# Optimization experiments

Hardware: AMD Instinct MI355X
Metric: run time of the kernel (lower is better)

## Reference

```python
import jax, jax.numpy as jnp
import numpy as np

BETA = 0.25


def setup_inputs() -> dict:
    key = jax.random.key(0)
    k1, k2 = jax.random.split(key)
    B, W, H, C = 32, 64, 64, 64
    K = 512
    x = jax.random.normal(k1, (B, W, H, C), dtype=jnp.float32)
    # original uses random_uniform_initializer(0, 1)
    embedding = jax.random.uniform(k2, (K, C), dtype=jnp.float32)
    return {"x": x, "embedding": embedding}


def reference(x, embedding):
    B, W, H, C = x.shape
    K = embedding.shape[0]
    flat = x.reshape(-1, C)  # (N, C), N = B*W*H
    # squared L2 distance, expanded form (same math as sum((flat - emb)^2, -1))
    # avoids materializing the (N, K, C) tiled tensor of the original
    x2 = jnp.sum(flat * flat, axis=-1, keepdims=True)          # (N, 1)
    e2 = jnp.sum(embedding * embedding, axis=-1)               # (K,)
    cross = jnp.einsum('nc,kc->nk', flat, embedding)           # (N, K)
    dist = x2 - 2.0 * cross + e2[None, :]                      # (N, K)
    idx = jnp.argmin(dist, axis=-1).reshape(B, W, H)           # (B, W, H)
    quantized = embedding[idx]                                 # (B, W, H, C)
    embedding_loss = jnp.mean((jax.lax.stop_gradient(x) - quantized) ** 2)
    encoding_loss = jnp.mean((x - jax.lax.stop_gradient(quantized)) ** 2)
    loss = embedding_loss + BETA * encoding_loss
    # straight-through estimator
    quantized_ste = x + jax.lax.stop_gradient(quantized - x)
    return quantized_ste, loss
```

## Files before the change

### kernel.cpp

```cpp
#include <hip/hip_runtime.h>


#define C_DIM 64
#define K_EMB 512
#define KCH   (K_EMB / 2)
#define NVEC (32 * 64 * 64)
#define BLK 512
#define NPB 256
#define GRID (NVEC / NPB)
#define KTC 16
#define NT 2

typedef __attribute__((ext_vector_type(8))) short bf16x8;
typedef __attribute__((ext_vector_type(4))) float f32x4;

#define WS_E2   0
#define WS_EHI  4096
#define WS_ELO  (4096 + 65536)
#define WS_PART (4096 + 2 * 65536)

__device__ inline unsigned short f2bf(float f) {
    unsigned u = __float_as_uint(f);
    u += 0x7FFF + ((u >> 16) & 1);
    return (unsigned short)(u >> 16);
}
__device__ inline float bf2f(unsigned short h) {
    return __uint_as_float(((unsigned)h) << 16);
}
__device__ inline bool lessidx(float s, int i, float t, int j) {
    return (s < t) || (s == t && i < j);
}

__global__ __launch_bounds__(512) void vq_prep(const float* __restrict__ emb,
                                               float* __restrict__ e2,
                                               short* __restrict__ ehi,
                                               short* __restrict__ elo) {
    const int t = blockIdx.x * 512 + threadIdx.x;
    const int l = t & 63;
    const int kt2 = t >> 6;
    const int row = (kt2 >> 1) * 16 + (l & 15);
    const int cb  = (kt2 & 1) * 32 + (l >> 4) * 8;
    const float* src = emb + row * C_DIM + cb;
    bf16x8 vh, vl;
#pragma unroll
    for (int j = 0; j < 8; ++j) {
        float v = -2.0f * src[j];
        unsigned short h = f2bf(v);
        float hf = bf2f(h);
        unsigned short q = f2bf(v - hf);
        vh[j] = (short)h;
        vl[j] = (short)q;
    }
    *(bf16x8*)(ehi + (size_t)t * 8) = vh;
    *(bf16x8*)(elo + (size_t)t * 8) = vl;

    if (t < K_EMB) {
        const float* r = emb + t * C_DIM;
        float s = 0.f;
#pragma unroll
        for (int c = 0; c < C_DIM; ++c) s += r[c] * r[c];
        e2[t] = s;
    }
}

__global__ __launch_bounds__(BLK, 4) void vq_main(
    const float* __restrict__ x,
    const float* __restrict__ emb,
    const float* __restrict__ e2g,
    const short* __restrict__ ehi_g,
    const short* __restrict__ elo_g,
    float* __restrict__ out,
    double* __restrict__ partials)
{
    __shared__ __align__(16) short s_hi[KCH * C_DIM];
    __shared__ __align__(16) short s_lo[KCH * C_DIM];
    __shared__ __align__(16) float s_e2[K_EMB];
    __shared__ double s_wsum[BLK / 64];

    const int tid  = threadIdx.x;
    const int lane = tid & 63;
    const int wid  = tid >> 6;
    const int lr   = lane & 15;
    const int lh   = lane >> 4;
    const int nbase = blockIdx.x * NPB + wid * 32;

    float4 xr[8];
#pragma unroll
    for (int nt = 0; nt < NT; ++nt) {
        const float* xp = x + (size_t)(nbase + nt * 16 + lr) * C_DIM;
#pragma unroll
        for (int s = 0; s < 2; ++s) {
            xr[nt * 4 + s * 2 + 0] = *(const float4*)(xp + s * 32 + lh * 8);
            xr[nt * 4 + s * 2 + 1] = *(const float4*)(xp + s * 32 + lh * 8 + 4);
        }
    }

    if (tid < K_EMB) s_e2[tid] = e2g[tid];
    {
        const float4* srch = (const float4*)ehi_g;
        const float4* srcl = (const float4*)elo_g;
        float4* dsth = (float4*)s_hi;
        float4* dstl = (float4*)s_lo;
#pragma unroll
        for (int i = 0; i < 4; ++i) dsth[tid + i * BLK] = srch[tid + i * BLK];
#pragma unroll
        for (int i = 0; i < 4; ++i) dstl[tid + i * BLK] = srcl[tid + i * BLK];
    }
    __syncthreads();

    bf16x8 xh[NT][2], xl[NT][2];
    float x2p[NT];
#pragma unroll
    for (int nt = 0; nt < NT; ++nt) {
        x2p[nt] = 0.f;
#pragma unroll
        for (int s = 0; s < 2; ++s) {
            float4 a = xr[nt * 4 + s * 2 + 0];
            float4 b = xr[nt * 4 + s * 2 + 1];
            float vv[8] = {a.x, a.y, a.z, a.w, b.x, b.y, b.z, b.w};
#pragma unroll
            for (int j = 0; j < 8; ++j) {
                float v = vv[j];
                x2p[nt] += v * v;
                unsigned short h = f2bf(v);
                float hf = bf2f(h);
                unsigned short q = f2bf(v - hf);
                xh[nt][s][j] = (short)h;
                xl[nt][s][j] = (short)q;
            }
        }
    }

    float pb1[NT] = {1e30f, 1e30f}, pb2[NT] = {1e30f, 1e30f};

#pragma unroll 1
    for (int ch = 0; ch < 2; ++ch) {
        if (ch == 1) {
            __syncthreads();
            const float4* srch = (const float4*)ehi_g + 2048;
            const float4* srcl = (const float4*)elo_g + 2048;
            float4* dsth = (float4*)s_hi;
            float4* dstl = (float4*)s_lo;
#pragma unroll
            for (int i = 0; i < 4; ++i) dsth[tid + i * BLK] = srch[tid + i * BLK];
#pragma unroll
            for (int i = 0; i < 4; ++i) dstl[tid + i * BLK] = srcl[tid + i * BLK];
            __syncthreads();
        }
        const int ktb = ch * KTC;
        const bf16x8* hb = (const bf16x8*)s_hi + lane;
        const bf16x8* lb = (const bf16x8*)s_lo + lane;

#pragma unroll 2
        for (int kt = 0; kt < KTC; ++kt) {
            bf16x8 ah0 = hb[kt * 128], ah1 = hb[kt * 128 + 64];
            bf16x8 al0 = lb[kt * 128], al1 = lb[kt * 128 + 64];
            float4 ev = *(const float4*)(s_e2 + (ktb + kt) * 16 + lh * 4);

            f32x4 h0 = {ev.x, ev.y, ev.z, ev.w};
            f32x4 h1 = h0;
            f32x4 p0 = {0.f, 0.f, 0.f, 0.f};
            f32x4 p1 = p0, q0 = p0, q1 = p0;

            h0 = __builtin_amdgcn_mfma_f32_16x16x32_bf16(ah0, xh[0][0], h0, 0, 0, 0);
            h1 = __builtin_amdgcn_mfma_f32_16x16x32_bf16(ah0, xh[1][0], h1, 0, 0, 0);
            p0 = __builtin_amdgcn_mfma_f32_16x16x32_bf16(al0, xh[0][0], p0, 0, 0, 0);
            p1 = __builtin_amdgcn_mfma_f32_16x16x32_bf16(al0, xh[1][0], p1, 0, 0, 0);
            q0 = __builtin_amdgcn_mfma_f32_16x16x32_bf16(ah0, xl[0][0], q0, 0, 0, 0);
            q1 = __builtin_amdgcn_mfma_f32_16x16x32_bf16(ah0, xl[1][0], q1, 0, 0, 0);
            h0 = __builtin_amdgcn_mfma_f32_16x16x32_bf16(ah1, xh[0][1], h0, 0, 0, 0);
            h1 = __builtin_amdgcn_mfma_f32_16x16x32_bf16(ah1, xh[1][1], h1, 0, 0, 0);
            p0 = __builtin_amdgcn_mfma_f32_16x16x32_bf16(al1, xh[0][1], p0, 0, 0, 0);
            p1 = __builtin_amdgcn_mfma_f32_16x16x32_bf16(al1, xh[1][1], p1, 0, 0, 0);
            q0 = __builtin_amdgcn_mfma_f32_16x16x32_bf16(ah1, xl[0][1], q0, 0, 0, 0);
            q1 = __builtin_amdgcn_mfma_f32_16x16x32_bf16(ah1, xl[1][1], q1, 0, 0, 0);

            f32x4 s0 = (h0 + p0) + q0;
            f32x4 s1 = (h1 + p1) + q1;

            const unsigned kb4 = (unsigned)((ktb + kt) * 4);
#define PACKMIN(ACC, NTI)                                                          \
            {                                                                      \
                unsigned u0 = ((__float_as_uint(ACC[0]) + 64u) & 0xFFFFFF80u) | (kb4 + 0); \
                unsigned u1 = ((__float_as_uint(ACC[1]) + 64u) & 0xFFFFFF80u) | (kb4 + 1); \
                unsigned u2 = ((__float_as_uint(ACC[2]) + 64u) & 0xFFFFFF80u) | (kb4 + 2); \
                unsigned u3 = ((__float_as_uint(ACC[3]) + 64u) & 0xFFFFFF80u) | (kb4 + 3); \
                float f0 = __uint_as_float(u0), f1 = __uint_as_float(u1);          \
                float f2 = __uint_as_float(u2), f3 = __uint_as_float(u3);          \
                float lo = fminf(f0, f1), hi = fmaxf(f0, f1);                      \
                pb2[NTI] = fminf(fminf(pb2[NTI], fmaxf(pb1[NTI], lo)), hi);        \
                pb1[NTI] = fminf(pb1[NTI], lo);                                    \
                lo = fminf(f2, f3); hi = fmaxf(f2, f3);                            \
                pb2[NTI] = fminf(fminf(pb2[NTI], fmaxf(pb1[NTI], lo)), hi);        \
                pb1[NTI] = fminf(pb1[NTI], lo);                                    \
            }
            PACKMIN(s0, 0)
            PACKMIN(s1, 1)
#undef PACKMIN
        }
    }

    double dsum = 0.0;
#pragma unroll
    for (int nt = 0; nt < NT; ++nt) {
        unsigned u1 = __float_as_uint(pb1[nt]);
        unsigned u2 = __float_as_uint(pb2[nt]);
        int loc1 = u1 & 127, loc2 = u2 & 127;
        float b1 = __uint_as_float(u1 & 0xFFFFFF80u);
        float b2 = __uint_as_float(u2 & 0xFFFFFF80u);
        int i1 = ((loc1 >> 2) << 4) + lh * 4 + (loc1 & 3);
        int i2 = ((loc2 >> 2) << 4) + lh * 4 + (loc2 & 3);
        float xx = x2p[nt];
#pragma unroll
        for (int off = 16; off <= 32; off <<= 1) {
            float ob1 = __shfl_xor(b1, off, 64);
            int   oi1 = __shfl_xor(i1, off, 64);
            float ob2 = __shfl_xor(b2, off, 64);
            int   oi2 = __shfl_xor(i2, off, 64);
            float oxx = __shfl_xor(xx, off, 64);
            xx += oxx;
            bool to = lessidx(ob1, oi1, b1, i1);
            float w1 = to ? ob1 : b1;  int wi1 = to ? oi1 : i1;
            float l1 = to ? b1 : ob1;  int li1 = to ? i1 : oi1;
            float c2 = to ? ob2 : b2;  int ci2 = to ? oi2 : i2;
            bool t2 = lessidx(l1, li1, c2, ci2);
            b1 = w1; i1 = wi1;
            b2 = t2 ? l1 : c2; i2 = t2 ? li1 : ci2;
        }

        int bw = i1;
        if (lane < 16) {
            double md;
            if (b2 - b1 < 1.2e-2f) {
                const int n = nbase + nt * 16 + lane;
                const float4* xq = (const float4*)(x + (size_t)n * C_DIM);
                const float4* p1 = (const float4*)(emb + (size_t)i1 * C_DIM);
                const float4* p2 = (const float4*)(emb + (size_t)i2 * C_DIM);
                double s1 = 0.0, s2 = 0.0;
#pragma unroll
                for (int i = 0; i < 16; ++i) {
                    float4 xv = xq[i]; float4 a = p1[i]; float4 bq = p2[i];
                    double d;
                    d = (double)xv.x - (double)a.x;  s1 = fma(d, d, s1);
                    d = (double)xv.y - (double)a.y;  s1 = fma(d, d, s1);
                    d = (double)xv.z - (double)a.z;  s1 = fma(d, d, s1);
                    d = (double)xv.w - (double)a.w;  s1 = fma(d, d, s1);
                    d = (double)xv.x - (double)bq.x; s2 = fma(d, d, s2);
                    d = (double)xv.y - (double)bq.y; s2 = fma(d, d, s2);
                    d = (double)xv.z - (double)bq.z; s2 = fma(d, d, s2);
                    d = (double)xv.w - (double)bq.w; s2 = fma(d, d, s2);
                }
                if (s2 < s1 || (s1 == s2 && i2 < i1)) { bw = i2; md = s2; }
                else                                   { md = s1; }
            } else {
                md = (double)xx + (double)b1;
            }
            dsum += md;
        }

        {
            const int v  = lane >> 2;
            const int c0 = lane & 3;
            const int w  = __shfl(bw, v);
            const size_t rowb = ((size_t)(nbase + nt * 16 + v)) * 16;
            const float4* ep = (const float4*)emb + (size_t)w * 16;
            float4* op = (float4*)out;
#pragma unroll
            for (int it = 0; it < 4; ++it) op[rowb + c0 + it * 4] = ep[c0 + it * 4];
        }
    }

#pragma unroll
    for (int off = 1; off <= 8; off <<= 1) dsum += __shfl_xor(dsum, off, 64);
    if (lane == 0) s_wsum[wid] = dsum;
    __syncthreads();
    if (tid == 0) {
        double t = 0.0;
#pragma unroll
        for (int i = 0; i < BLK / 64; ++i) t += s_wsum[i];
        partials[blockIdx.x] = t;
    }
}

__global__ __launch_bounds__(512) void vq_finalize(const double* __restrict__ partials,
                                                   float* __restrict__ out) {
    double v = partials[threadIdx.x];
#pragma unroll
    for (int off = 32; off; off >>= 1) v += __shfl_down(v, off, 64);
    __shared__ double ls[8];
    const int lane = threadIdx.x & 63;
    const int wid  = threadIdx.x >> 6;
    if (lane == 0) ls[wid] = v;
    __syncthreads();
    if (threadIdx.x == 0) {
        double t = 0.0;
#pragma unroll
        for (int i = 0; i < 8; ++i) t += ls[i];
        double mean = t / (double)((size_t)NVEC * C_DIM);
        out[(size_t)NVEC * C_DIM] = (float)(1.25 * mean);
    }
}

extern "C" void kernel_launch(void* const* d_in, const int* in_sizes, int n_in,
                              void* d_out, int out_size, void* d_ws, size_t ws_size,
                              hipStream_t stream) {
    const float* x   = (const float*)d_in[0];
    const float* emb = (const float*)d_in[1];
    float* out = (float*)d_out;

    float*  e2       = (float*)((char*)d_ws + WS_E2);
    short*  ehi      = (short*)((char*)d_ws + WS_EHI);
    short*  elo      = (short*)((char*)d_ws + WS_ELO);
    double* partials = (double*)((char*)d_ws + WS_PART);

    vq_prep<<<8, 512, 0, stream>>>(emb, e2, ehi, elo);
    vq_main<<<GRID, BLK, 0, stream>>>(x, emb, e2, ehi, elo, out, partials);
    vq_finalize<<<1, 512, 0, stream>>>(partials, out);
}
```

Baseline: 53.19 us.

## Switch to fp16 split-x MFMA with single embedding copy and larger per-wave tile

The codebook is now a single fp16 copy of -2*emb kept entirely in LDS, replacing the bf16 hi/lo pair that was loaded in two chunks. Only x is split into hi and lo halves, which cuts the MFMAs per tile from 3 products to 2. Each wave now covers 64 vectors (NT=4) and blocks drop to 256 threads, so embedding fragments are reused across more MFMAs and the mid-kernel resync and reload go away. The near-tie fallback is widened and now runs in parallel across lanes with fp64 distances, to make up for fp16 losing exponent range and precision. This costs 64KB of LDS per block, which lowers occupancy, and a wider fallback window sends more vectors down the exact path.

```diff
diff --git a/kernel.cpp b/kernel.cpp
--- a/kernel.cpp
+++ b/kernel.cpp
@@ -3,56 +3,55 @@
 
 #define C_DIM 64
 #define K_EMB 512
-#define KCH   (K_EMB / 2)
 #define NVEC (32 * 64 * 64)
-#define BLK 512
+#define BLK 256
+#define VPW 64
 #define NPB 256
 #define GRID (NVEC / NPB)
-#define KTC 16
-#define NT 2
-
-typedef __attribute__((ext_vector_type(8))) short bf16x8;
+#define KT (K_EMB / 16)
+#define NT 4
+#define WINF 2.5e-2f
+
+typedef __attribute__((ext_vector_type(8))) _Float16 f16x8;
 typedef __attribute__((ext_vector_type(4))) float f32x4;
 
 #define WS_E2   0
-#define WS_EHI  4096
-#define WS_ELO  (4096 + 65536)
-#define WS_PART (4096 + 2 * 65536)
-
-__device__ inline unsigned short f2bf(float f) {
-    unsigned u = __float_as_uint(f);
-    u += 0x7FFF + ((u >> 16) & 1);
-    return (unsigned short)(u >> 16);
-}
-__device__ inline float bf2f(unsigned short h) {
-    return __uint_as_float(((unsigned)h) << 16);
-}
+#define WS_AE   4096
+#define WS_PART (4096 + 65536)
+
 __device__ inline bool lessidx(float s, int i, float t, int j) {
     return (s < t) || (s == t && i < j);
 }
 
+__device__ __forceinline__ double dist64(const float4* __restrict__ xq,
+                                         const float* __restrict__ ep) {
+    const float4* e4 = (const float4*)ep;
+    double s = 0.0;
+#pragma unroll
+    for (int i = 0; i < 16; ++i) {
+        float4 xv = xq[i]; float4 a = e4[i];
+        double d;
+        d = (double)xv.x - (double)a.x; s = fma(d, d, s);
+        d = (double)xv.y - (double)a.y; s = fma(d, d, s);
+        d = (double)xv.z - (double)a.z; s = fma(d, d, s);
+        d = (double)xv.w - (double)a.w; s = fma(d, d, s);
+    }
+    return s;
+}
+
 __global__ __launch_bounds__(512) void vq_prep(const float* __restrict__ emb,
                                                float* __restrict__ e2,
-                                               short* __restrict__ ehi,
-                                               short* __restrict__ elo) {
+                                               short* __restrict__ ae) {
     const int t = blockIdx.x * 512 + threadIdx.x;
     const int l = t & 63;
     const int kt2 = t >> 6;
     const int row = (kt2 >> 1) * 16 + (l & 15);
     const int cb  = (kt2 & 1) * 32 + (l >> 4) * 8;
     const float* src = emb + row * C_DIM + cb;
-    bf16x8 vh, vl;
-#pragma unroll
-    for (int j = 0; j < 8; ++j) {
-        float v = -2.0f * src[j];
-        unsigned short h = f2bf(v);
-        float hf = bf2f(h);
-        unsigned short q = f2bf(v - hf);
-        vh[j] = (short)h;
-        vl[j] = (short)q;
-    }
-    *(bf16x8*)(ehi + (size_t)t * 8) = vh;
-    *(bf16x8*)(elo + (size_t)t * 8) = vl;
+    f16x8 vh;
+#pragma unroll
+    for (int j = 0; j < 8; ++j) vh[j] = (_Float16)(-2.0f * src[j]);
+    *(f16x8*)(ae + (size_t)t * 8) = vh;
 
     if (t < K_EMB) {
         const float* r = emb + t * C_DIM;
@@ -63,17 +62,15 @@
     }
 }
 
-__global__ __launch_bounds__(BLK, 4) void vq_main(
+__global__ __launch_bounds__(BLK, 2) void vq_main(
     const float* __restrict__ x,
     const float* __restrict__ emb,
     const float* __restrict__ e2g,
-    const short* __restrict__ ehi_g,
-    const short* __restrict__ elo_g,
+    const short* __restrict__ ae_g,
     float* __restrict__ out,
     double* __restrict__ partials)
 {
-    __shared__ __align__(16) short s_hi[KCH * C_DIM];
-    __shared__ __align__(16) short s_lo[KCH * C_DIM];
+    __shared__ __align__(16) short s_ae[K_EMB * C_DIM];
     __shared__ __align__(16) float s_e2[K_EMB];
     __shared__ double s_wsum[BLK / 64];
 
@@ -82,9 +79,9 @@
     const int wid  = tid >> 6;
     const int lr   = lane & 15;
     const int lh   = lane >> 4;
-    const int nbase = blockIdx.x * NPB + wid * 32;
-
-    float4 xr[8];
+    const int nbase = blockIdx.x * NPB + wid * VPW;
+
+    float4 xr[NT * 4];
 #pragma unroll
     for (int nt = 0; nt < NT; ++nt) {
         const float* xp = x + (size_t)(nbase + nt * 16 + lr) * C_DIM;
@@ -95,20 +92,17 @@
         }
     }
 
-    if (tid < K_EMB) s_e2[tid] = e2g[tid];
     {
-        const float4* srch = (const float4*)ehi_g;
-        const float4* srcl = (const float4*)elo_g;
-        float4* dsth = (float4*)s_hi;
-        float4* dstl = (float4*)s_lo;
-#pragma unroll
-        for (int i = 0; i < 4; ++i) dsth[tid + i * BLK] = srch[tid + i * BLK];
-#pragma unroll
-        for (int i = 0; i < 4; ++i) dstl[tid + i * BLK] = srcl[tid + i * BLK];
+        const float4* srca = (const float4*)ae_g;
+        float4* dsta = (float4*)s_ae;
+#pragma unroll
+        for (int i = 0; i < 16; ++i) dsta[tid + i * BLK] = srca[tid + i * BLK];
+        s_e2[tid] = e2g[tid];
+        s_e2[tid + 256] = e2g[tid + 256];
     }
     __syncthreads();
 
-    bf16x8 xh[NT][2], xl[NT][2];
+    f16x8 xh[NT][2], xl[NT][2];
     float x2p[NT];
 #pragma unroll
     for (int nt = 0; nt < NT; ++nt) {
@@ -122,81 +116,52 @@
             for (int j = 0; j < 8; ++j) {
                 float v = vv[j];
                 x2p[nt] += v * v;
-                unsigned short h = f2bf(v);
-                float hf = bf2f(h);
-                unsigned short q = f2bf(v - hf);
-                xh[nt][s][j] = (short)h;
-                xl[nt][s][j] = (short)q;
+                _Float16 h = (_Float16)v;
+                xh[nt][s][j] = h;
+                xl[nt][s][j] = (_Float16)(v - (float)h);
             }
         }
     }
 
-    float pb1[NT] = {1e30f, 1e30f}, pb2[NT] = {1e30f, 1e30f};
-
-#pragma unroll 1
-    for (int ch = 0; ch < 2; ++ch) {
-        if (ch == 1) {
-            __syncthreads();
-            const float4* srch = (const float4*)ehi_g + 2048;
-            const float4* srcl = (const float4*)elo_g + 2048;
-            float4* dsth = (float4*)s_hi;
-            float4* dstl = (float4*)s_lo;
-#pragma unroll
-            for (int i = 0; i < 4; ++i) dsth[tid + i * BLK] = srch[tid + i * BLK];
-#pragma unroll
-            for (int i = 0; i < 4; ++i) dstl[tid + i * BLK] = srcl[tid + i * BLK];
-            __syncthreads();
-        }
-        const int ktb = ch * KTC;
-        const bf16x8* hb = (const bf16x8*)s_hi + lane;
-        const bf16x8* lb = (const bf16x8*)s_lo + lane;
+    float pb1[NT] = {1e30f, 1e30f, 1e30f, 1e30f};
+    float pb2[NT] = {1e30f, 1e30f, 1e30f, 1e30f};
+    const f16x8* ab = (const f16x8*)s_ae + lane;
 
 #pragma unroll 2
-        for (int kt = 0; kt < KTC; ++kt) {
-            bf16x8 ah0 = hb[kt * 128], ah1 = hb[kt * 128 + 64];
-            bf16x8 al0 = lb[kt * 128], al1 = lb[kt * 128 + 64];
-            float4 ev = *(const float4*)(s_e2 + (ktb + kt) * 16 + lh * 4);
-
-            f32x4 h0 = {ev.x, ev.y, ev.z, ev.w};
-            f32x4 h1 = h0;
-            f32x4 p0 = {0.f, 0.f, 0.f, 0.f};
-            f32x4 p1 = p0, q0 = p0, q1 = p0;
-
-            h0 = __builtin_amdgcn_mfma_f32_16x16x32_bf16(ah0, xh[0][0], h0, 0, 0, 0);
-            h1 = __builtin_amdgcn_mfma_f32_16x16x32_bf16(ah0, xh[1][0], h1, 0, 0, 0);
-            p0 = __builtin_amdgcn_mfma_f32_16x16x32_bf16(al0, xh[0][0], p0, 0, 0, 0);
-            p1 = __builtin_amdgcn_mfma_f32_16x16x32_bf16(al0, xh[1][0], p1, 0, 0, 0);
-            q0 = __builtin_amdgcn_mfma_f32_16x16x32_bf16(ah0, xl[0][0], q0, 0, 0, 0);
-            q1 = __builtin_amdgcn_mfma_f32_16x16x32_bf16(ah0, xl[1][0], q1, 0, 0, 0);
-            h0 = __builtin_amdgcn_mfma_f32_16x16x32_bf16(ah1, xh[0][1], h0, 0, 0, 0);
-            h1 = __builtin_amdgcn_mfma_f32_16x16x32_bf16(ah1, xh[1][1], h1, 0, 0, 0);
-            p0 = __builtin_amdgcn_mfma_f32_16x16x32_bf16(al1, xh[0][1], p0, 0, 0, 0);
-            p1 = __builtin_amdgcn_mfma_f32_16x16x32_bf16(al1, xh[1][1], p1, 0, 0, 0);
-            q0 = __builtin_amdgcn_mfma_f32_16x16x32_bf16(ah1, xl[0][1], q0, 0, 0, 0);
-            q1 = __builtin_amdgcn_mfma_f32_16x16x32_bf16(ah1, xl[1][1], q1, 0, 0, 0);
-
-            f32x4 s0 = (h0 + p0) + q0;
-            f32x4 s1 = (h1 + p1) + q1;
-
-            const unsigned kb4 = (unsigned)((ktb + kt) * 4);
-#define PACKMIN(ACC, NTI)                                                          \
-            {                                                                      \
-                unsigned u0 = ((__float_as_uint(ACC[0]) + 64u) & 0xFFFFFF80u) | (kb4 + 0); \
-                unsigned u1 = ((__float_as_uint(ACC[1]) + 64u) & 0xFFFFFF80u) | (kb4 + 1); \
-                unsigned u2 = ((__float_as_uint(ACC[2]) + 64u) & 0xFFFFFF80u) | (kb4 + 2); \
-                unsigned u3 = ((__float_as_uint(ACC[3]) + 64u) & 0xFFFFFF80u) | (kb4 + 3); \
-                float f0 = __uint_as_float(u0), f1 = __uint_as_float(u1);          \
-                float f2 = __uint_as_float(u2), f3 = __uint_as_float(u3);          \
-                float lo = fminf(f0, f1), hi = fmaxf(f0, f1);                      \
-                pb2[NTI] = fminf(fminf(pb2[NTI], fmaxf(pb1[NTI], lo)), hi);        \
-                pb1[NTI] = fminf(pb1[NTI], lo);                                    \
-                lo = fminf(f2, f3); hi = fmaxf(f2, f3);                            \
-                pb2[NTI] = fminf(fminf(pb2[NTI], fmaxf(pb1[NTI], lo)), hi);        \
-                pb1[NTI] = fminf(pb1[NTI], lo);                                    \
-            }
-            PACKMIN(s0, 0)
-            PACKMIN(s1, 1)
-#undef PACKMIN
+    for (int kt = 0; kt < KT; ++kt) {
+        f16x8 a0 = ab[kt * 128], a1 = ab[kt * 128 + 64];
+        f32x4 ev = *(const f32x4*)(s_e2 + kt * 16 + lh * 4);
+        f32x4 c[NT];
+#pragma unroll
+        for (int nt = 0; nt < NT; ++nt) c[nt] = ev;
+#pragma unroll
+        for (int nt = 0; nt < NT; ++nt)
+            c[nt] = __builtin_amdgcn_mfma_f32_16x16x32_f16(a0, xh[nt][0], c[nt], 0, 0, 0);
+#pragma unroll
+        for (int nt = 0; nt < NT; ++nt)
+            c[nt] = __builtin_amdgcn_mfma_f32_16x16x32_f16(a1, xh[nt][1], c[nt], 0, 0, 0);
+#pragma unroll
+        for (int nt = 0; nt < NT; ++nt)
+            c[nt] = __builtin_amdgcn_mfma_f32_16x16x32_f16(a0, xl[nt][0], c[nt], 0, 0, 0);
+#pragma unroll
+        for (int nt = 0; nt < NT; ++nt)
+            c[nt] = __builtin_amdgcn_mfma_f32_16x16x32_f16(a1, xl[nt][1], c[nt], 0, 0, 0);
+
+        const unsigned kb4 = (unsigned)(kt * 4);
+#pragma unroll
+        for (int nt = 0; nt < NT; ++nt) {
+            unsigned q0 = (__float_as_uint(c[nt][0]) & 0xFFFFFF80u) | (kb4 + 0);
+            unsigned q1 = (__float_as_uint(c[nt][1]) & 0xFFFFFF80u) | (kb4 + 1);
+            unsigned q2 = (__float_as_uint(c[nt][2]) & 0xFFFFFF80u) | (kb4 + 2);
+            unsigned q3 = (__float_as_uint(c[nt][3]) & 0xFFFFFF80u) | (kb4 + 3);
+            float f0 = __uint_as_float(q0), f1 = __uint_as_float(q1);
+            float f2 = __uint_as_float(q2), f3 = __uint_as_float(q3);
+            float lo = fminf(f0, f1), hi = fmaxf(f0, f1);
+            pb2[nt] = fminf(fminf(pb2[nt], fmaxf(pb1[nt], lo)), hi);
+            pb1[nt] = fminf(pb1[nt], lo);
+            lo = fminf(f2, f3); hi = fmaxf(f2, f3);
+            pb2[nt] = fminf(fminf(pb2[nt], fmaxf(pb1[nt], lo)), hi);
+            pb1[nt] = fminf(pb1[nt], lo);
         }
     }
 
@@ -210,53 +175,57 @@
         float b2 = __uint_as_float(u2 & 0xFFFFFF80u);
         int i1 = ((loc1 >> 2) << 4) + lh * 4 + (loc1 & 3);
         int i2 = ((loc2 >> 2) << 4) + lh * 4 + (loc2 & 3);
+        const float os1 = b1, os2 = b2;
+        const int   oi1 = i1, oi2 = i2;
+
         float xx = x2p[nt];
 #pragma unroll
         for (int off = 16; off <= 32; off <<= 1) {
             float ob1 = __shfl_xor(b1, off, 64);
-            int   oi1 = __shfl_xor(i1, off, 64);
+            int   oI1 = __shfl_xor(i1, off, 64);
             float ob2 = __shfl_xor(b2, off, 64);
-            int   oi2 = __shfl_xor(i2, off, 64);
+            int   oI2 = __shfl_xor(i2, off, 64);
             float oxx = __shfl_xor(xx, off, 64);
             xx += oxx;
-            bool to = lessidx(ob1, oi1, b1, i1);
-            float w1 = to ? ob1 : b1;  int wi1 = to ? oi1 : i1;
-            float l1 = to ? b1 : ob1;  int li1 = to ? i1 : oi1;
-            float c2 = to ? ob2 : b2;  int ci2 = to ? oi2 : i2;
+            bool to = lessidx(ob1, oI1, b1, i1);
+            float w1 = to ? ob1 : b1;  int wi1 = to ? oI1 : i1;
+            float l1 = to ? b1 : ob1;  int li1 = to ? i1 : oI1;
+            float c2 = to ? ob2 : b2;  int ci2 = to ? oI2 : i2;
             bool t2 = lessidx(l1, li1, c2, ci2);
             b1 = w1; i1 = wi1;
             b2 = t2 ? l1 : c2; i2 = t2 ? li1 : ci2;
         }
 
-        int bw = i1;
-        if (lane < 16) {
-            double md;
-            if (b2 - b1 < 1.2e-2f) {
-                const int n = nbase + nt * 16 + lane;
-                const float4* xq = (const float4*)(x + (size_t)n * C_DIM);
-                const float4* p1 = (const float4*)(emb + (size_t)i1 * C_DIM);
-                const float4* p2 = (const float4*)(emb + (size_t)i2 * C_DIM);
-                double s1 = 0.0, s2 = 0.0;
-#pragma unroll
-                for (int i = 0; i < 16; ++i) {
-                    float4 xv = xq[i]; float4 a = p1[i]; float4 bq = p2[i];
-                    double d;
-                    d = (double)xv.x - (double)a.x;  s1 = fma(d, d, s1);
-                    d = (double)xv.y - (double)a.y;  s1 = fma(d, d, s1);
-                    d = (double)xv.z - (double)a.z;  s1 = fma(d, d, s1);
-                    d = (double)xv.w - (double)a.w;  s1 = fma(d, d, s1);
-                    d = (double)xv.x - (double)bq.x; s2 = fma(d, d, s2);
-                    d = (double)xv.y - (double)bq.y; s2 = fma(d, d, s2);
-                    d = (double)xv.z - (double)bq.z; s2 = fma(d, d, s2);
-                    d = (double)xv.w - (double)bq.w; s2 = fma(d, d, s2);
-                }
-                if (s2 < s1 || (s1 == s2 && i2 < i1)) { bw = i2; md = s2; }
-                else                                   { md = s1; }
-            } else {
-                md = (double)xx + (double)b1;
+        const int n = nbase + nt * 16 + lr;
+        const float4* xq = (const float4*)(x + (size_t)n * C_DIM);
+
+        int bw;
+        double md;
+        if (b2 - b1 < WINF) {
+            bool f1 = (os1 <= b1 + WINF);
+            bool f2 = (os2 <= b1 + WINF);
+            double d1 = 1e300, d2 = 1e300;
+            if (f1) d1 = dist64(xq, emb + (size_t)oi1 * C_DIM);
+            if (f2) d2 = dist64(xq, emb + (size_t)oi2 * C_DIM);
+            bool t = (d2 < d1) || (d2 == d1 && oi2 < oi1);
+            double dl = t ? d2 : d1;
+            int    il = t ? oi2 : oi1;
+#pragma unroll
+            for (int off = 16; off <= 32; off <<= 1) {
+                double od = __shfl_xor(dl, off, 64);
+                int    oi = __shfl_xor(il, off, 64);
+                bool tk = (od < dl) || (od == dl && oi < il);
+                dl = tk ? od : dl;
+                il = tk ? oi : il;
             }
-            dsum += md;
-        }
+            bw = il;
+            md = dl;
+        } else {
+            bw = i1;
+            md = (double)xx + (double)b1;
+        }
+
+        if (lane < 16) dsum += md;
 
         {
             const int v  = lane >> 2;
@@ -309,11 +278,10 @@
     float* out = (float*)d_out;
 
     float*  e2       = (float*)((char*)d_ws + WS_E2);
-    short*  ehi      = (short*)((char*)d_ws + WS_EHI);
-    short*  elo      = (short*)((char*)d_ws + WS_ELO);
+    short*  ae       = (short*)((char*)d_ws + WS_AE);
     double* partials = (double*)((char*)d_ws + WS_PART);
 
-    vq_prep<<<8, 512, 0, stream>>>(emb, e2, ehi, elo);
-    vq_main<<<GRID, BLK, 0, stream>>>(x, emb, e2, ehi, elo, out, partials);
+    vq_prep<<<8, 512, 0, stream>>>(emb, e2, ae);
+    vq_main<<<GRID, BLK, 0, stream>>>(x, emb, e2, ae, out, partials);
     vq_finalize<<<1, 512, 0, stream>>>(partials, out);
 }
```

Result: faster. 43.98 us, median of 2 (-17.3%).
